# Kernel optimization log

Measured on AMD Instinct MI355X. Metric: run time of the kernel, lower is better.

Reference implementation:

```python
import jax, jax.numpy as jnp
import numpy as np


def _mux(sel, a, b):
    # VecMUX semantics: sel==1 -> a, sel==0 -> b (linear soft-mux matches spiking impl)
    return sel * a + (1.0 - sel) * b


def setup_inputs() -> dict:
    key = jax.random.key(0)
    # FP64 bit-spike tensor: [S | E10..E0 | M51..M0] along last dim (64 lanes).
    x = jax.random.uniform(key, (512, 2048, 64), dtype=jnp.float32)
    return {"x": x}


def reference(x):
    sign = x[..., 0:1]
    e10 = x[..., 1:2]    # exponent MSB (E10)
    e0 = x[..., 11:12]   # exponent LSB (E0)
    m51 = x[..., 12:13]  # mantissa MSB
    m50 = x[..., 13:14]
    ones = jnp.ones_like(m51)
    zeros = jnp.zeros_like(m51)
    # E==1024 -> mod4 = 2 + M51 ; E==1025 -> mod4 = 2*M51 + M50 ; selected by E0
    b0_high = _mux(e0, m50, m51)
    b1_high = _mux(e0, m51, ones)
    # E10==0 -> value in {0,1}: mod4 = E0 (bit0), bit1 = 0
    b0 = _mux(e10, b0_high, e0)
    b1 = _mux(e10, b1_high, zeros)
    result = jnp.concatenate([b1, b0], axis=-1)  # [..., 2]
    return (result, sign)
```

## Files before the change

### kernel.cpp

```cpp
#include <hip/hip_runtime.h>


__global__ void spike_extract_kernel(const float* __restrict__ x,
                                     float* __restrict__ result,
                                     float* __restrict__ sign_out,
                                     int nrows) {
    int row = blockIdx.x * blockDim.x + threadIdx.x;
    if (row >= nrows) return;

    const float4* base = reinterpret_cast<const float4*>(x + (size_t)row * 64);
    float4 c0 = base[0];
    float4 c2 = base[2];
    float4 c3 = base[3];

    float s   = c0.x;
    float e10 = c0.y;
    float e0  = c2.w;
    float m51 = c3.x;
    float m50 = c3.y;

    float b0_high = fmaf(e0, m50 - m51, m51);
    float b1_high = fmaf(e0, m51 - 1.0f, 1.0f);
    float b0      = fmaf(e10, b0_high - e0, e0);
    float b1      = e10 * b1_high;

    reinterpret_cast<float2*>(result)[row] = make_float2(b1, b0);
    sign_out[row] = s;
}

extern "C" void kernel_launch(void* const* d_in, const int* in_sizes, int n_in,
                              void* d_out, int out_size, void* d_ws, size_t ws_size,
                              hipStream_t stream) {
    const float* x = (const float*)d_in[0];
    float* out = (float*)d_out;

    int nrows = in_sizes[0] / 64;
    float* result = out;
    float* sign_out = out + (size_t)nrows * 2;

    const int block = 256;
    const int grid = (nrows + block - 1) / block;
    spike_extract_kernel<<<grid, block, 0, stream>>>(x, result, sign_out, nrows);
}
```

Before: 26.30 us.

## Use four lanes per row with coalesced float4 loads and shuffles

Each group of four lanes now reads the first 64 bytes of one row as contiguous float4s, and wave shuffles gather the needed bits to the lanes that compute and write. A grid-stride loop over a fixed grid of 2048 blocks replaces one thread per row. The aim is more contiguous memory access per wave than the old strided per-thread loads. It adds shuffle overhead, leaves the ragged tail unhandled when nrows is not a multiple of 16, and caps parallelism at a fixed grid size.

```diff
diff --git a/kernel.cpp b/kernel.cpp
--- a/kernel.cpp
+++ b/kernel.cpp
@@ -1,31 +1,40 @@
 #include <hip/hip_runtime.h>
 
 
-__global__ void spike_extract_kernel(const float* __restrict__ x,
-                                     float* __restrict__ result,
-                                     float* __restrict__ sign_out,
-                                     int nrows) {
-    int row = blockIdx.x * blockDim.x + threadIdx.x;
-    if (row >= nrows) return;
+__global__ void spike_extract_coop(const float* __restrict__ x,
+                                   float* __restrict__ result,
+                                   float* __restrict__ sign_out,
+                                   int nrows) {
+    const int lane = threadIdx.x & 63;
+    const int sub  = lane & 3;
+    const int rl   = lane >> 2;
+    const int waves_per_block = blockDim.x >> 6;
+    const int wave_id = blockIdx.x * waves_per_block + (threadIdx.x >> 6);
+    const int total_waves = gridDim.x * waves_per_block;
+    const int ngroups = nrows >> 4;
 
-    const float4* base = reinterpret_cast<const float4*>(x + (size_t)row * 64);
-    float4 c0 = base[0];
-    float4 c2 = base[2];
-    float4 c3 = base[3];
+    for (int g = wave_id; g < ngroups; g += total_waves) {
+        const int row = (g << 4) + rl;
+        const float4 c = *reinterpret_cast<const float4*>(
+            x + ((size_t)row << 6) + (sub << 2));
 
-    float s   = c0.x;
-    float e10 = c0.y;
-    float e0  = c2.w;
-    float m51 = c3.x;
-    float m50 = c3.y;
+        const int base = lane & ~3;
+        const float e0  = __shfl(c.w, base + 2, 64);
+        const float m51 = __shfl(c.x, base + 3, 64);
+        const float m50 = __shfl(c.y, base + 3, 64);
+        const float s   = __shfl(c.x, base,     64);
 
-    float b0_high = fmaf(e0, m50 - m51, m51);
-    float b1_high = fmaf(e0, m51 - 1.0f, 1.0f);
-    float b0      = fmaf(e10, b0_high - e0, e0);
-    float b1      = e10 * b1_high;
-
-    reinterpret_cast<float2*>(result)[row] = make_float2(b1, b0);
-    sign_out[row] = s;
+        if (sub == 0) {
+            const float e10 = c.y;
+            float b0_high = fmaf(e0, m50 - m51, m51);
+            float b1_high = fmaf(e0, m51 - 1.0f, 1.0f);
+            float b0      = fmaf(e10, b0_high - e0, e0);
+            float b1      = e10 * b1_high;
+            reinterpret_cast<float2*>(result)[row] = make_float2(b1, b0);
+        } else if (sub == 1) {
+            sign_out[row] = s;
+        }
+    }
 }
 
 extern "C" void kernel_launch(void* const* d_in, const int* in_sizes, int n_in,
@@ -39,6 +48,6 @@
     float* sign_out = out + (size_t)nrows * 2;
 
     const int block = 256;
-    const int grid = (nrows + block - 1) / block;
-    spike_extract_kernel<<<grid, block, 0, stream>>>(x, result, sign_out, nrows);
+    const int grid = 2048;
+    spike_extract_coop<<<grid, block, 0, stream>>>(x, result, sign_out, nrows);
 }
```

New measurement: 27.30 us. +3.8%, slower.
